# Kernel optimization log

Hardware: AMD Instinct MI355X
Metric: run time of the kernel (lower is better)

## Reference

```python
import jax, jax.numpy as jnp
import numpy as np

INIT_IN = 32      # init_input_dim (raw feature dim of x)
D = 128           # output_dim == init_output_dim
IN_DIM = 2 * D + INIT_IN  # input_dim = 288
NUM_LAYERS = 4    # loop runs num_layers-1 = 3 rounds
NV = 50000        # num variables
NC = 50000        # num constraints
DEG = 16          # padded neighbor list length


def _linear_params(key, out_dim, in_dim):
    k1, k2 = jax.random.split(key)
    bound = 1.0 / np.sqrt(in_dim)
    W = jax.random.uniform(k1, (out_dim, in_dim), minval=-bound, maxval=bound, dtype=jnp.float32)
    b = jax.random.uniform(k2, (out_dim,), minval=-bound, maxval=bound, dtype=jnp.float32)
    return W, b


def setup_inputs() -> dict:
    key = jax.random.key(0)
    ks = jax.random.split(key, 8)
    x = jax.random.normal(ks[0], (NV + NC, INIT_IN), dtype=jnp.float32)
    var_constr_index = jax.random.randint(ks[1], (NV, DEG), 0, NC).astype(jnp.int64)
    constr_var_index = jax.random.randint(ks[2], (NC, DEG), 0, NV).astype(jnp.int64)
    W_iv, b_iv = _linear_params(ks[3], D, INIT_IN)
    W_ic, b_ic = _linear_params(ks[4], D, INIT_IN)
    W_v, b_v = _linear_params(ks[5], D, IN_DIM)
    W_c, b_c = _linear_params(ks[6], D, IN_DIM)
    W_q, b_q = _linear_params(ks[7], 1, 2 * D)
    return dict(x=x, var_constr_index=var_constr_index, constr_var_index=constr_var_index,
                W_iv=W_iv, b_iv=b_iv, W_ic=W_ic, b_ic=b_ic,
                W_v=W_v, b_v=b_v, W_c=W_c, b_c=b_c, W_q=W_q, b_q=b_q)


def reference(x, var_constr_index, constr_var_index,
              W_iv, b_iv, W_ic, b_ic, W_v, b_v, W_c, b_c, W_q, b_q):
    nv = var_constr_index.shape[0]
    var_feat = x[:nv]          # [NV, INIT_IN]
    con_feat = x[nv:]          # [NC, INIT_IN]
    # layer zero init
    lv = var_feat @ W_iv.T + b_iv   # [NV, D]
    lc = con_feat @ W_ic.T + b_ic   # [NC, D]
    zeros = jnp.zeros((1, D), dtype=lv.dtype)
    for _ in range(1, NUM_LAYERS):
        lv_pad = jnp.concatenate([lv, zeros], axis=0)  # -1 pad idx -> zeros row
        lc_pad = jnp.concatenate([lc, zeros], axis=0)
        # constraint update: gather variable neighbors, sum, fuse with linear
        c_agg = lv_pad[constr_var_index].sum(axis=1)   # [NC, D]
        lc_new = jnp.concatenate([c_agg, lc, con_feat], axis=1) @ W_c.T + b_c
        # variable update uses OLD (pre-update) constraint features (lc_pad)
        v_agg = lc_pad[var_constr_index].sum(axis=1)   # [NV, D]
        lv = jnp.concatenate([v_agg, lv, var_feat], axis=1) @ W_v.T + b_v
        lc = lc_new
    # embedding_Q: global sum of variable features broadcast to each variable
    g = lv.sum(axis=0, keepdims=True)                  # [1, D]
    g = jnp.broadcast_to(g, lv.shape)                  # [NV, D]
    Q = jnp.concatenate([g, lv], axis=1) @ W_q.T + b_q # [NV, 1]
    return Q
```

## Files before the change

kernel.cpp:

```cpp
#include <hip/hip_runtime.h>

#define NVV 50000
#define NCC 50000
#define DD 128
#define FIN 32
#define INDIM 288
#define DEG 16

typedef unsigned short u16;
typedef unsigned char u8;
typedef unsigned int u32;
typedef __attribute__((ext_vector_type(8))) short short8;
typedef __attribute__((ext_vector_type(4))) float f32x4;
typedef __attribute__((ext_vector_type(2))) float f32x2;

constexpr int NT = 256;
constexpr int GRID_HALF = 782;

__device__ __forceinline__ float b2f(u16 b) {
  union { u32 u; float f; } v; v.u = ((u32)b) << 16; return v.f;
}
__device__ __forceinline__ u16 f2b(float f) {
  union { float f; u32 u; } v; v.f = f;
  u32 u = v.u + 0x7FFFu + ((v.u >> 16) & 1u);
  return (u16)(u >> 16);
}
__device__ __forceinline__ float bits2f(u32 u) {
  union { u32 u; float f; } v; v.u = u; return v.f;
}
__device__ __forceinline__ u32 pack2(float a, float b) {
  return (u32)f2b(a) | ((u32)f2b(b) << 16);
}
__device__ __forceinline__ u8 f2fp8(float f) {
  return (u8)(__builtin_amdgcn_cvt_pk_fp8_f32(f, f, 0, false) & 0xFF);
}

__device__ __forceinline__ void dma16(const void* g, void* l) {
  __builtin_amdgcn_global_load_lds(
      (__attribute__((address_space(1))) void*)g,
      (__attribute__((address_space(3))) void*)l, 16, 0, 0);
}

__global__ __launch_bounds__(NT) void swizzle_all(
    const float* __restrict__ Wv, const float* __restrict__ Wc,
    const float* __restrict__ Wiv, const float* __restrict__ Wic,
    u16* __restrict__ Wvsw, u16* __restrict__ Wcsw,
    u16* __restrict__ Wivsw, u16* __restrict__ Wicsw)
{
  int t = blockIdx.x * NT + threadIdx.x;
  if (t >= 10240) return;
  const float* W; u16* out; int f; int indim;
  if (t < 4608)       { W = Wv;  out = Wvsw;  f = t;        indim = INDIM; }
  else if (t < 9216)  { W = Wc;  out = Wcsw;  f = t - 4608; indim = INDIM; }
  else if (t < 9728)  { W = Wiv; out = Wivsw; f = t - 9216; indim = FIN; }
  else                { W = Wic; out = Wicsw; f = t - 9728; indim = FIN; }
  int lane = f & 63, nt = (f >> 6) & 7, kt = f >> 9;
  int li = lane & 15, quad = lane >> 4;
  const float* src = W + (size_t)(nt * 16 + li) * indim + kt * 32 + quad * 8;
  float4 a = *(const float4*)src, b = *(const float4*)(src + 4);
  u32 o[4] = { pack2(a.x, a.y), pack2(a.z, a.w), pack2(b.x, b.y), pack2(b.z, b.w) };
  *(int4*)(out + (size_t)f * 8) = *(int4*)o;
}

__global__ __launch_bounds__(NT) void init_fused(
    const float* __restrict__ x,
    const u16* __restrict__ Wivsw, const u16* __restrict__ Wicsw,
    const float* __restrict__ b_iv, const float* __restrict__ b_ic,
    u16* __restrict__ lv0, u16* __restrict__ lc0,
    u8* __restrict__ lv08, u8* __restrict__ lc08,
    u16* __restrict__ xvb, u16* __restrict__ xcb)
{
  __shared__ char smem8[4 * 2048];
  const int bid = blockIdx.x;
  const bool isC = bid >= GRID_HALF;
  const int lb = isC ? bid - GRID_HALF : bid;
  const float* xs = x + (isC ? (size_t)NVV * FIN : 0);
  const u16* Wsw = isC ? Wicsw : Wivsw;
  const float* bias = isC ? b_ic : b_iv;
  u16* out  = isC ? lc0 : lv0;
  u8*  out8 = isC ? lc08 : lv08;
  u16* feat = isC ? xcb : xvb;
  const int nrows = isC ? NCC : NVV;

  const int t = threadIdx.x;
  const int r0 = lb * 64;

  {
    const int row = r0 + (t >> 2);
    if (row < nrows) {
      const float* src = xs + (size_t)row * FIN + (t & 3) * 8;
      float4 a = *(const float4*)src, b = *(const float4*)(src + 4);
      u32 o[4] = { pack2(a.x, a.y), pack2(a.z, a.w), pack2(b.x, b.y), pack2(b.z, b.w) };
      *(int4*)(feat + (size_t)row * FIN + (t & 3) * 8) = *(int4*)o;
    }
  }

  const int wave = t >> 6, l = t & 63;
  const int quad = l >> 4, li = l & 15;
  const int r0w = r0 + wave * 16;
  int rowm = r0w + li;
  if (rowm >= nrows) rowm = nrows - 1;

  short8 afrag;
  {
    const float* src = xs + (size_t)rowm * FIN + quad * 8;
    float4 a = *(const float4*)src, b = *(const float4*)(src + 4);
    u32 o[4] = { pack2(a.x, a.y), pack2(a.z, a.w), pack2(b.x, b.y), pack2(b.z, b.w) };
    afrag = *(short8*)o;
  }

  f32x4 acc[8];
#pragma unroll
  for (int nt = 0; nt < 8; ++nt) acc[nt] = (f32x4){0.f, 0.f, 0.f, 0.f};
#pragma unroll
  for (int nt = 0; nt < 8; ++nt) {
    short8 b = *(const short8*)(Wsw + (size_t)(nt * 64 + l) * 8);
    acc[nt] = __builtin_amdgcn_mfma_f32_16x16x32_bf16(afrag, b, acc[nt], 0, 0, 0);
  }

  u8* s8 = (u8*)(smem8 + wave * 2048);
  const int rbase = r0w + quad * 4;
#pragma unroll
  for (int nt = 0; nt < 8; ++nt) {
    const int col = nt * 16 + li;
    const float bv = bias[col];
#pragma unroll
    for (int i = 0; i < 4; ++i) {
      const int row = rbase + i;
      float v = acc[nt][i] + bv;
      if (row < nrows) out[(size_t)row * DD + col] = f2b(v);
      s8[(quad * 4 + i) * 128 + col] = f2fp8(v);
    }
  }
  asm volatile("s_waitcnt lgkmcnt(0)" ::: "memory");
  if (r0w < nrows) {
    const char* s8c = (const char*)s8 + l * 32;
    char* g8 = (char*)out8 + (size_t)r0w * 128 + l * 32;
#pragma unroll
    for (int c = 0; c < 2; ++c) *(int4*)(g8 + c * 16) = *(const int4*)(s8c + c * 16);
  }
}

__device__ __forceinline__ void issue_group16(const char* gp, int offj, char* slotbase) {
  const char* rp = gp + (size_t)(u32)offj;
#pragma unroll
  for (int k2 = 0; k2 < 4; ++k2)
    dma16(rp + k2 * 64, slotbase + k2 * 1024);
}
__device__ __forceinline__ void consume_slot16(const char* sb, float (&sagg)[4][8]) {
#pragma unroll
  for (int k2 = 0; k2 < 4; ++k2) {
    int4 v = *(const int4*)(sb + k2 * 1024);
    const u32* w = (const u32*)&v;
#pragma unroll
    for (int p = 0; p < 4; ++p) {
      sagg[k2][2 * p]     += bits2f(w[p] << 16);
      sagg[k2][2 * p + 1] += bits2f(w[p] & 0xFFFF0000u);
    }
  }
}
__device__ __forceinline__ void issue_group8(const char* gp, int offj, char* slotbase) {
  const char* rp = gp + (size_t)(u32)offj;
  dma16(rp, slotbase);
  dma16(rp + 64, slotbase + 1024);
}
__device__ __forceinline__ void consume_slot8(const char* slot, int li, int quad,
                                              float (&sagg)[4][8]) {
  const int c2 = quad >> 1, half = quad & 1;
#pragma unroll
  for (int kt = 0; kt < 4; ++kt) {
    int4 v = *(const int4*)(slot + (2 * kt + c2) * 256 + li * 16);
    u32 w0 = half ? (u32)v.z : (u32)v.x;
    u32 w1 = half ? (u32)v.w : (u32)v.y;
    f32x2 a0 = __builtin_amdgcn_cvt_pk_f32_fp8(w0, false);
    f32x2 a1 = __builtin_amdgcn_cvt_pk_f32_fp8(w0, true);
    f32x2 a2 = __builtin_amdgcn_cvt_pk_f32_fp8(w1, false);
    f32x2 a3 = __builtin_amdgcn_cvt_pk_f32_fp8(w1, true);
    sagg[kt][0] += a0.x; sagg[kt][1] += a0.y;
    sagg[kt][2] += a1.x; sagg[kt][3] += a1.y;
    sagg[kt][4] += a2.x; sagg[kt][5] += a2.y;
    sagg[kt][6] += a3.x; sagg[kt][7] += a3.y;
  }
}

template <bool F8, bool W8, bool GACC>
__device__ __forceinline__ void layer_body(
    const void* __restrict__ gsrc, const u16* __restrict__ self,
    const u16* __restrict__ feat, const int* __restrict__ idx,
    const u16* __restrict__ Wsw, const float* __restrict__ bias,
    u16* __restrict__ out, u8* __restrict__ out8, float* __restrict__ g,
    int nrows, int bid, int t, char* smem)
{
  const int wave = t >> 6, l = t & 63;
  const int quad = l >> 4, li = l & 15;
  const int r0w = bid * 64 + wave * 16;

  int4 iv;
  {
    int rload = r0w + (l >> 2);
    if (rload >= nrows) rload = nrows - 1;
    iv = *(const int4*)(idx + (size_t)rload * DEG + (l & 3) * 4);
  }
  int off[DEG];
#pragma unroll
  for (int j = 0; j < DEG; ++j) {
    int comp = ((j & 3) == 0) ? iv.x : ((j & 3) == 1) ? iv.y : ((j & 3) == 2) ? iv.z : iv.w;
    off[j] = __shfl(comp, (li << 2) + (j >> 2)) << (F8 ? 7 : 8);
  }

  int rowm = r0w + li;
  if (rowm >= nrows) rowm = nrows - 1;

  f32x4 acc[8];
#pragma unroll
  for (int nt = 0; nt < 8; ++nt) acc[nt] = (f32x4){0.f, 0.f, 0.f, 0.f};

  {
    short8 a = *(const short8*)(feat + (size_t)rowm * FIN + quad * 8);
#pragma unroll
    for (int nt = 0; nt < 8; ++nt) {
      short8 b = *(const short8*)(Wsw + (size_t)((8 * 8 + nt) * 64 + l) * 8);
      acc[nt] = __builtin_amdgcn_mfma_f32_16x16x32_bf16(a, b, acc[nt], 0, 0, 0);
    }
  }
#pragma unroll
  for (int k2 = 0; k2 < 4; ++k2) {
    short8 a = *(const short8*)(self + (size_t)rowm * DD + k2 * 32 + quad * 8);
#pragma unroll
    for (int nt = 0; nt < 8; ++nt) {
      short8 b = *(const short8*)(Wsw + (size_t)(((4 + k2) * 8 + nt) * 64 + l) * 8);
      acc[nt] = __builtin_amdgcn_mfma_f32_16x16x32_bf16(a, b, acc[nt], 0, 0, 0);
    }
  }

  float sagg[4][8];
#pragma unroll
  for (int k2 = 0; k2 < 4; ++k2)
#pragma unroll
    for (int p = 0; p < 8; ++p) sagg[k2][p] = 0.f;

  asm volatile("s_waitcnt vmcnt(0)" ::: "memory");

  char* wb;
  if constexpr (F8) {
    wb = smem + wave * 8192;
    const char* gp = (const char*)gsrc + quad * 16;
    issue_group8(gp, off[0], wb);
    issue_group8(gp, off[1], wb + 2048);
    issue_group8(gp, off[2], wb + 4096);
    issue_group8(gp, off[3], wb + 6144);
#define R8_STEP(J, IJ)                                               \
    asm volatile("s_waitcnt vmcnt(6)" ::: "memory");                 \
    consume_slot8(wb + ((J) & 3) * 2048, li, quad, sagg);            \
    asm volatile("s_waitcnt lgkmcnt(0)" ::: "memory");               \
    issue_group8(gp, off[IJ], wb + ((J) & 3) * 2048);
#define R8_TAIL(J, VN)                                               \
    asm volatile("s_waitcnt vmcnt(" #VN ")" ::: "memory");           \
    consume_slot8(wb + ((J) & 3) * 2048, li, quad, sagg);
    R8_STEP(0, 4)  R8_STEP(1, 5)  R8_STEP(2, 6)  R8_STEP(3, 7)
    R8_STEP(4, 8)  R8_STEP(5, 9)  R8_STEP(6, 10) R8_STEP(7, 11)
    R8_STEP(8, 12) R8_STEP(9, 13) R8_STEP(10, 14) R8_STEP(11, 15)
    R8_TAIL(12, 6) R8_TAIL(13, 4) R8_TAIL(14, 2)  R8_TAIL(15, 0)
#undef R8_STEP
#undef R8_TAIL
  } else {
    wb = smem + wave * 16384;
    const char* gp = (const char*)gsrc + quad * 16;
    issue_group16(gp, off[0], wb);
    issue_group16(gp, off[1], wb + 4096);
    issue_group16(gp, off[2], wb + 8192);
    issue_group16(gp, off[3], wb + 12288);
#define R16_STEP(J, IJ)                                              \
    asm volatile("s_waitcnt vmcnt(12)" ::: "memory");                \
    consume_slot16(wb + ((J) & 3) * 4096 + l * 16, sagg);            \
    asm volatile("s_waitcnt lgkmcnt(0)" ::: "memory");               \
    issue_group16(gp, off[IJ], wb + ((J) & 3) * 4096);
#define R16_TAIL(J, VN)                                              \
    asm volatile("s_waitcnt vmcnt(" #VN ")" ::: "memory");           \
    consume_slot16(wb + ((J) & 3) * 4096 + l * 16, sagg);
    R16_STEP(0, 4)  R16_STEP(1, 5)  R16_STEP(2, 6)  R16_STEP(3, 7)
    R16_STEP(4, 8)  R16_STEP(5, 9)  R16_STEP(6, 10) R16_STEP(7, 11)
    R16_STEP(8, 12) R16_STEP(9, 13) R16_STEP(10, 14) R16_STEP(11, 15)
    R16_TAIL(12, 12) R16_TAIL(13, 8) R16_TAIL(14, 4) R16_TAIL(15, 0)
#undef R16_STEP
#undef R16_TAIL
  }

#pragma unroll
  for (int k2 = 0; k2 < 4; ++k2) {
    u32 a_bits[4];
#pragma unroll
    for (int p = 0; p < 4; ++p) a_bits[p] = pack2(sagg[k2][2 * p], sagg[k2][2 * p + 1]);
    short8 a = *(short8*)a_bits;
#pragma unroll
    for (int nt = 0; nt < 8; ++nt) {
      short8 b = *(const short8*)(Wsw + (size_t)((k2 * 8 + nt) * 64 + l) * 8);
      acc[nt] = __builtin_amdgcn_mfma_f32_16x16x32_bf16(a, b, acc[nt], 0, 0, 0);
    }
  }

  asm volatile("s_waitcnt lgkmcnt(0)" ::: "memory");
  u8* s8 = (u8*)wb;
  const int rbase = r0w + quad * 4;
  float colsum[8];
#pragma unroll
  for (int nt = 0; nt < 8; ++nt) {
    const int col = nt * 16 + li;
    const float bv = bias[col];
    colsum[nt] = 0.f;
#pragma unroll
    for (int i = 0; i < 4; ++i) {
      const int row = rbase + i;
      float v = acc[nt][i] + bv;
      if (row < nrows) {
        out[(size_t)row * DD + col] = f2b(v);
        if constexpr (GACC) colsum[nt] += v;
      }
      if constexpr (W8) s8[(quad * 4 + i) * 128 + col] = f2fp8(v);
    }
  }
  if constexpr (W8) {
    asm volatile("s_waitcnt lgkmcnt(0)" ::: "memory");
    if (r0w < nrows) {
      const char* s8c = (const char*)s8 + l * 32;
      char* g8 = (char*)out8 + (size_t)r0w * 128 + l * 32;
#pragma unroll
      for (int c = 0; c < 2; ++c) *(int4*)(g8 + c * 16) = *(const int4*)(s8c + c * 16);
    }
  }

  if constexpr (GACC) {
#pragma unroll
    for (int nt = 0; nt < 8; ++nt) {
      colsum[nt] += __shfl_xor(colsum[nt], 16);
      colsum[nt] += __shfl_xor(colsum[nt], 32);
    }
    __syncthreads();
    float* gsum = (float*)smem;
    if (quad == 0) {
#pragma unroll
      for (int nt = 0; nt < 8; ++nt) gsum[wave * 128 + nt * 16 + li] = colsum[nt];
    }
    __syncthreads();
    if (t < 128) {
      float tot = gsum[t] + gsum[128 + t] + gsum[256 + t] + gsum[384 + t];
      atomicAdd(&g[t], tot);
    }
  }
}

template <bool F8, bool W8, bool GACC>
__global__ __launch_bounds__(NT, 2) void layer_merged(
    const void* gsrcC, const u16* selfC, const u16* featC, const int* idxC,
    const u16* WswC, const float* biasC, u16* outC, u8* out8C, int nrowsC,
    const void* gsrcV, const u16* selfV, const u16* featV, const int* idxV,
    const u16* WswV, const float* biasV, u16* outV, u8* out8V, int nrowsV,
    float* g, int c_blocks)
{
  __shared__ char smem[F8 ? 32768 : 65536];
  const int bid = blockIdx.x;
  const int t = threadIdx.x;
  if (bid < c_blocks)
    layer_body<F8, W8, GACC>(gsrcC, selfC, featC, idxC, WswC, biasC, outC, out8C,
                             g, nrowsC, bid, t, smem);
  else
    layer_body<F8, W8, GACC>(gsrcV, selfV, featV, idxV, WswV, biasV, outV, out8V,
                             g, nrowsV, bid - c_blocks, t, smem);
}

__global__ void zero_g(float* g) { g[threadIdx.x] = 0.f; }

__global__ __launch_bounds__(NT) void final_kernel(
    const u16* __restrict__ lv, const float* __restrict__ g,
    const float* __restrict__ Wq, const float* __restrict__ bq,
    float* __restrict__ out)
{
  const int t = threadIdx.x, wave = t >> 6, l = t & 63;
  const float2 wg = *(const float2*)(Wq + 2 * l);
  const float2 wl = *(const float2*)(Wq + DD + 2 * l);
  const float2 gv = *(const float2*)(g + 2 * l);
  float q = wg.x * gv.x + wg.y * gv.y;
#pragma unroll
  for (int off = 32; off; off >>= 1) q += __shfl_down(q, off);
  const float qg = __shfl(q, 0) + bq[0];

  const int r0w = blockIdx.x * 64 + wave * 16;
#pragma unroll
  for (int i = 0; i < 16; ++i) {
    const int r = r0w + i;
    if (r >= NVV) break;
    u32 v = *(const u32*)(lv + (size_t)r * DD + 2 * l);
    float p = wl.x * b2f((u16)(v & 0xFFFF)) + wl.y * b2f((u16)(v >> 16));
#pragma unroll
    for (int off = 32; off; off >>= 1) p += __shfl_down(p, off);
    if (l == 0) out[r] = qg + p;
  }
}

extern "C" void kernel_launch(void* const* d_in, const int* in_sizes, int n_in,
                              void* d_out, int out_size, void* d_ws, size_t ws_size,
                              hipStream_t stream) {
  const float* x    = (const float*)d_in[0];
  const int*   vci  = (const int*)d_in[1];
  const int*   cvi  = (const int*)d_in[2];
  const float* W_iv = (const float*)d_in[3];
  const float* b_iv = (const float*)d_in[4];
  const float* W_ic = (const float*)d_in[5];
  const float* b_ic = (const float*)d_in[6];
  const float* W_v  = (const float*)d_in[7];
  const float* b_v  = (const float*)d_in[8];
  const float* W_c  = (const float*)d_in[9];
  const float* b_c  = (const float*)d_in[10];
  const float* W_q  = (const float*)d_in[11];
  const float* b_q  = (const float*)d_in[12];
  float* out = (float*)d_out;

  float* g = (float*)d_ws;
  u16* base = (u16*)((char*)d_ws + 512);
  const size_t nodef = (size_t)NVV * DD;
  u16* xb    = base;
  u16* Wvsw  = xb + (size_t)(NVV + NCC) * FIN;
  u16* Wcsw  = Wvsw + (size_t)DD * INDIM;
  u16* Wivsw = Wcsw + (size_t)DD * INDIM;
  u16* Wicsw = Wivsw + (size_t)DD * FIN;
  u16* lv0   = Wicsw + (size_t)DD * FIN;
  u16* lc0   = lv0 + nodef;
  u16* lv1   = lc0 + nodef;
  u16* lc1   = lv1 + nodef;
  u8*  lv08  = (u8*)(lc1 + nodef);
  u8*  lc08  = lv08 + nodef;
  u8*  lv18  = lc08 + nodef;
  u8*  lc18  = lv18 + nodef;
  u16* xvb   = xb;
  u16* xcb   = xb + (size_t)NVV * FIN;

  dim3 blk(NT);

  swizzle_all<<<40, blk, 0, stream>>>(W_v, W_c, W_iv, W_ic, Wvsw, Wcsw, Wivsw, Wicsw);
  init_fused<<<2 * GRID_HALF, blk, 0, stream>>>(x, Wivsw, Wicsw, b_iv, b_ic,
                                                lv0, lc0, lv08, lc08, xvb, xcb);
  zero_g<<<1, 128, 0, stream>>>(g);

  layer_merged<true, true, false><<<2 * GRID_HALF, blk, 0, stream>>>(
      lv08, lc0, xcb, cvi, Wcsw, b_c, lc1, lc18, NCC,
      lc08, lv0, xvb, vci, Wvsw, b_v, lv1, lv18, NVV, g, GRID_HALF);
  layer_merged<true, false, false><<<2 * GRID_HALF, blk, 0, stream>>>(
      lv18, lc1, xcb, cvi, Wcsw, b_c, lc0, nullptr, NCC,
      lc18, lv1, xvb, vci, Wvsw, b_v, lv0, nullptr, NVV, g, GRID_HALF);
  layer_merged<false, false, true><<<GRID_HALF, blk, 0, stream>>>(
      lv0, lc0, xcb, cvi, Wcsw, b_c, lc1, nullptr, NCC,
      lc0, lv0, xvb, vci, Wvsw, b_v, lv1, nullptr, NVV, g, 0);

  final_kernel<<<GRID_HALF, blk, 0, stream>>>(lv1, g, W_q, b_q, out);
}
```

Before: 325.7 us.

## Use fp8 gathers in last layer, stage stores via LDS with nontemporal writes

```diff
diff --git a/kernel.cpp b/kernel.cpp
--- a/kernel.cpp
+++ b/kernel.cpp
@@ -13,6 +13,7 @@
 typedef __attribute__((ext_vector_type(8))) short short8;
 typedef __attribute__((ext_vector_type(4))) float f32x4;
 typedef __attribute__((ext_vector_type(2))) float f32x2;
+typedef __attribute__((ext_vector_type(4))) unsigned int u32x4;
 
 constexpr int NT = 256;
 constexpr int GRID_HALF = 782;
@@ -40,15 +41,25 @@
       (__attribute__((address_space(1))) void*)g,
       (__attribute__((address_space(3))) void*)l, 16, 0, 0);
 }
+__device__ __forceinline__ short8 ntload8(const u16* p) {
+  return __builtin_nontemporal_load((const short8*)p);
+}
+__device__ __forceinline__ void ntstore16(void* p, u32x4 v) {
+  __builtin_nontemporal_store(v, (u32x4*)p);
+}
 
 __global__ __launch_bounds__(NT) void swizzle_all(
     const float* __restrict__ Wv, const float* __restrict__ Wc,
     const float* __restrict__ Wiv, const float* __restrict__ Wic,
     u16* __restrict__ Wvsw, u16* __restrict__ Wcsw,
-    u16* __restrict__ Wivsw, u16* __restrict__ Wicsw)
+    u16* __restrict__ Wivsw, u16* __restrict__ Wicsw, float* __restrict__ g)
 {
   int t = blockIdx.x * NT + threadIdx.x;
-  if (t >= 10240) return;
+  if (t >= 10240) {
+    int gi = t - 10240;
+    if (gi < 128) g[gi] = 0.f;
+    return;
+  }
   const float* W; u16* out; int f; int indim;
   if (t < 4608)       { W = Wv;  out = Wvsw;  f = t;        indim = INDIM; }
   else if (t < 9216)  { W = Wc;  out = Wcsw;  f = t - 4608; indim = INDIM; }
@@ -58,8 +69,8 @@
   int li = lane & 15, quad = lane >> 4;
   const float* src = W + (size_t)(nt * 16 + li) * indim + kt * 32 + quad * 8;
   float4 a = *(const float4*)src, b = *(const float4*)(src + 4);
-  u32 o[4] = { pack2(a.x, a.y), pack2(a.z, a.w), pack2(b.x, b.y), pack2(b.z, b.w) };
-  *(int4*)(out + (size_t)f * 8) = *(int4*)o;
+  u32x4 o = { pack2(a.x, a.y), pack2(a.z, a.w), pack2(b.x, b.y), pack2(b.z, b.w) };
+  *(u32x4*)(out + (size_t)f * 8) = o;
 }
 
 __global__ __launch_bounds__(NT) void init_fused(
@@ -70,7 +81,7 @@
     u8* __restrict__ lv08, u8* __restrict__ lc08,
     u16* __restrict__ xvb, u16* __restrict__ xcb)
 {
-  __shared__ char smem8[4 * 2048];
+  __shared__ char smem[4 * 8192];
   const int bid = blockIdx.x;
   const bool isC = bid >= GRID_HALF;
   const int lb = isC ? bid - GRID_HALF : bid;
@@ -90,8 +101,8 @@
     if (row < nrows) {
       const float* src = xs + (size_t)row * FIN + (t & 3) * 8;
       float4 a = *(const float4*)src, b = *(const float4*)(src + 4);
-      u32 o[4] = { pack2(a.x, a.y), pack2(a.z, a.w), pack2(b.x, b.y), pack2(b.z, b.w) };
-      *(int4*)(feat + (size_t)row * FIN + (t & 3) * 8) = *(int4*)o;
+      u32x4 o = { pack2(a.x, a.y), pack2(a.z, a.w), pack2(b.x, b.y), pack2(b.z, b.w) };
+      ntstore16(feat + (size_t)row * FIN + (t & 3) * 8, o);
     }
   }
 
@@ -105,8 +116,8 @@
   {
     const float* src = xs + (size_t)rowm * FIN + quad * 8;
     float4 a = *(const float4*)src, b = *(const float4*)(src + 4);
-    u32 o[4] = { pack2(a.x, a.y), pack2(a.z, a.w), pack2(b.x, b.y), pack2(b.z, b.w) };
-    afrag = *(short8*)o;
+    u32x4 o = { pack2(a.x, a.y), pack2(a.z, a.w), pack2(b.x, b.y), pack2(b.z, b.w) };
+    afrag = *(short8*)&o;
   }
 
   f32x4 acc[8];
@@ -118,47 +129,33 @@
     acc[nt] = __builtin_amdgcn_mfma_f32_16x16x32_bf16(afrag, b, acc[nt], 0, 0, 0);
   }
 
-  u8* s8 = (u8*)(smem8 + wave * 2048);
-  const int rbase = r0w + quad * 4;
+  char* wb = smem + wave * 8192;
+  u16* swt = (u16*)wb;
+  u8*  s8  = (u8*)(wb + 4096);
 #pragma unroll
   for (int nt = 0; nt < 8; ++nt) {
     const int col = nt * 16 + li;
     const float bv = bias[col];
 #pragma unroll
     for (int i = 0; i < 4; ++i) {
-      const int row = rbase + i;
       float v = acc[nt][i] + bv;
-      if (row < nrows) out[(size_t)row * DD + col] = f2b(v);
+      swt[(quad * 4 + i) * 128 + col] = f2b(v);
       s8[(quad * 4 + i) * 128 + col] = f2fp8(v);
     }
   }
   asm volatile("s_waitcnt lgkmcnt(0)" ::: "memory");
   if (r0w < nrows) {
+    const char* sc = (const char*)swt + l * 64;
+    char* g16 = (char*)out + (size_t)r0w * 256 + l * 64;
+#pragma unroll
+    for (int c = 0; c < 4; ++c) ntstore16(g16 + c * 16, *(const u32x4*)(sc + c * 16));
     const char* s8c = (const char*)s8 + l * 32;
     char* g8 = (char*)out8 + (size_t)r0w * 128 + l * 32;
 #pragma unroll
-    for (int c = 0; c < 2; ++c) *(int4*)(g8 + c * 16) = *(const int4*)(s8c + c * 16);
-  }
-}
-
-__device__ __forceinline__ void issue_group16(const char* gp, int offj, char* slotbase) {
-  const char* rp = gp + (size_t)(u32)offj;
-#pragma unroll
-  for (int k2 = 0; k2 < 4; ++k2)
-    dma16(rp + k2 * 64, slotbase + k2 * 1024);
-}
-__device__ __forceinline__ void consume_slot16(const char* sb, float (&sagg)[4][8]) {
-#pragma unroll
-  for (int k2 = 0; k2 < 4; ++k2) {
-    int4 v = *(const int4*)(sb + k2 * 1024);
-    const u32* w = (const u32*)&v;
-#pragma unroll
-    for (int p = 0; p < 4; ++p) {
-      sagg[k2][2 * p]     += bits2f(w[p] << 16);
-      sagg[k2][2 * p + 1] += bits2f(w[p] & 0xFFFF0000u);
-    }
-  }
-}
+    for (int c = 0; c < 2; ++c) ntstore16(g8 + c * 16, *(const u32x4*)(s8c + c * 16));
+  }
+}
+
 __device__ __forceinline__ void issue_group8(const char* gp, int offj, char* slotbase) {
   const char* rp = gp + (size_t)(u32)offj;
   dma16(rp, slotbase);
@@ -183,9 +180,9 @@
   }
 }
 
-template <bool F8, bool W8, bool GACC>
+template <bool GACC>
 __device__ __forceinline__ void layer_body(
-    const void* __restrict__ gsrc, const u16* __restrict__ self,
+    const u8* __restrict__ gsrc, const u16* __restrict__ self,
     const u16* __restrict__ feat, const int* __restrict__ idx,
     const u16* __restrict__ Wsw, const float* __restrict__ bias,
     u16* __restrict__ out, u8* __restrict__ out8, float* __restrict__ g,
@@ -205,7 +202,7 @@
 #pragma unroll
   for (int j = 0; j < DEG; ++j) {
     int comp = ((j & 3) == 0) ? iv.x : ((j & 3) == 1) ? iv.y : ((j & 3) == 2) ? iv.z : iv.w;
-    off[j] = __shfl(comp, (li << 2) + (j >> 2)) << (F8 ? 7 : 8);
+    off[j] = __shfl(comp, (li << 2) + (j >> 2)) << 7;
   }
 
   int rowm = r0w + li;
@@ -216,7 +213,7 @@
   for (int nt = 0; nt < 8; ++nt) acc[nt] = (f32x4){0.f, 0.f, 0.f, 0.f};
 
   {
-    short8 a = *(const short8*)(feat + (size_t)rowm * FIN + quad * 8);
+    short8 a = ntload8(feat + (size_t)rowm * FIN + quad * 8);
 #pragma unroll
     for (int nt = 0; nt < 8; ++nt) {
       short8 b = *(const short8*)(Wsw + (size_t)((8 * 8 + nt) * 64 + l) * 8);
@@ -225,7 +222,7 @@
   }
 #pragma unroll
   for (int k2 = 0; k2 < 4; ++k2) {
-    short8 a = *(const short8*)(self + (size_t)rowm * DD + k2 * 32 + quad * 8);
+    short8 a = ntload8(self + (size_t)rowm * DD + k2 * 32 + quad * 8);
 #pragma unroll
     for (int nt = 0; nt < 8; ++nt) {
       short8 b = *(const short8*)(Wsw + (size_t)(((4 + k2) * 8 + nt) * 64 + l) * 8);
@@ -241,50 +238,26 @@
 
   asm volatile("s_waitcnt vmcnt(0)" ::: "memory");
 
-  char* wb;
-  if constexpr (F8) {
-    wb = smem + wave * 8192;
-    const char* gp = (const char*)gsrc + quad * 16;
-    issue_group8(gp, off[0], wb);
-    issue_group8(gp, off[1], wb + 2048);
-    issue_group8(gp, off[2], wb + 4096);
-    issue_group8(gp, off[3], wb + 6144);
+  char* wb = smem + wave * 8192;
+  const char* gp = (const char*)gsrc + quad * 16;
+  issue_group8(gp, off[0], wb);
+  issue_group8(gp, off[1], wb + 2048);
+  issue_group8(gp, off[2], wb + 4096);
+  issue_group8(gp, off[3], wb + 6144);
 #define R8_STEP(J, IJ)                                               \
-    asm volatile("s_waitcnt vmcnt(6)" ::: "memory");                 \
-    consume_slot8(wb + ((J) & 3) * 2048, li, quad, sagg);            \
-    asm volatile("s_waitcnt lgkmcnt(0)" ::: "memory");               \
-    issue_group8(gp, off[IJ], wb + ((J) & 3) * 2048);
+  asm volatile("s_waitcnt vmcnt(6)" ::: "memory");                   \
+  consume_slot8(wb + ((J) & 3) * 2048, li, quad, sagg);              \
+  asm volatile("s_waitcnt lgkmcnt(0)" ::: "memory");                 \
+  issue_group8(gp, off[IJ], wb + ((J) & 3) * 2048);
 #define R8_TAIL(J, VN)                                               \
-    asm volatile("s_waitcnt vmcnt(" #VN ")" ::: "memory");           \
-    consume_slot8(wb + ((J) & 3) * 2048, li, quad, sagg);
-    R8_STEP(0, 4)  R8_STEP(1, 5)  R8_STEP(2, 6)  R8_STEP(3, 7)
-    R8_STEP(4, 8)  R8_STEP(5, 9)  R8_STEP(6, 10) R8_STEP(7, 11)
-    R8_STEP(8, 12) R8_STEP(9, 13) R8_STEP(10, 14) R8_STEP(11, 15)
-    R8_TAIL(12, 6) R8_TAIL(13, 4) R8_TAIL(14, 2)  R8_TAIL(15, 0)
+  asm volatile("s_waitcnt vmcnt(" #VN ")" ::: "memory");             \
+  consume_slot8(wb + ((J) & 3) * 2048, li, quad, sagg);
+  R8_STEP(0, 4)  R8_STEP(1, 5)  R8_STEP(2, 6)  R8_STEP(3, 7)
+  R8_STEP(4, 8)  R8_STEP(5, 9)  R8_STEP(6, 10) R8_STEP(7, 11)
+  R8_STEP(8, 12) R8_STEP(9, 13) R8_STEP(10, 14) R8_STEP(11, 15)
+  R8_TAIL(12, 6) R8_TAIL(13, 4) R8_TAIL(14, 2)  R8_TAIL(15, 0)
 #undef R8_STEP
 #undef R8_TAIL
-  } else {
-    wb = smem + wave * 16384;
-    const char* gp = (const char*)gsrc + quad * 16;
-    issue_group16(gp, off[0], wb);
-    issue_group16(gp, off[1], wb + 4096);
-    issue_group16(gp, off[2], wb + 8192);
-    issue_group16(gp, off[3], wb + 12288);
-#define R16_STEP(J, IJ)                                              \
-    asm volatile("s_waitcnt vmcnt(12)" ::: "memory");                \
-    consume_slot16(wb + ((J) & 3) * 4096 + l * 16, sagg);            \
-    asm volatile("s_waitcnt lgkmcnt(0)" ::: "memory");               \
-    issue_group16(gp, off[IJ], wb + ((J) & 3) * 4096);
-#define R16_TAIL(J, VN)                                              \
-    asm volatile("s_waitcnt vmcnt(" #VN ")" ::: "memory");           \
-    consume_slot16(wb + ((J) & 3) * 4096 + l * 16, sagg);
-    R16_STEP(0, 4)  R16_STEP(1, 5)  R16_STEP(2, 6)  R16_STEP(3, 7)
-    R16_STEP(4, 8)  R16_STEP(5, 9)  R16_STEP(6, 10) R16_STEP(7, 11)
-    R16_STEP(8, 12) R16_STEP(9, 13) R16_STEP(10, 14) R16_STEP(11, 15)
-    R16_TAIL(12, 12) R16_TAIL(13, 8) R16_TAIL(14, 4) R16_TAIL(15, 0)
-#undef R16_STEP
-#undef R16_TAIL
-  }
 
 #pragma unroll
   for (int k2 = 0; k2 < 4; ++k2) {
@@ -300,8 +273,9 @@
   }
 
   asm volatile("s_waitcnt lgkmcnt(0)" ::: "memory");
-  u8* s8 = (u8*)wb;
-  const int rbase = r0w + quad * 4;
+  u16* swt = (u16*)wb;
+  u8*  s8  = (u8*)(wb + 4096);
+  const bool wvalid = (r0w < nrows);
   float colsum[8];
 #pragma unroll
   for (int nt = 0; nt < 8; ++nt) {
@@ -310,26 +284,31 @@
     colsum[nt] = 0.f;
 #pragma unroll
     for (int i = 0; i < 4; ++i) {
-      const int row = rbase + i;
       float v = acc[nt][i] + bv;
-      if (row < nrows) {
-        out[(size_t)row * DD + col] = f2b(v);
-        if constexpr (GACC) colsum[nt] += v;
-      }
-      if constexpr (W8) s8[(quad * 4 + i) * 128 + col] = f2fp8(v);
-    }
-  }
-  if constexpr (W8) {
-    asm volatile("s_waitcnt lgkmcnt(0)" ::: "memory");
-    if (r0w < nrows) {
+      swt[(quad * 4 + i) * 128 + col] = f2b(v);
+      if (out8) s8[(quad * 4 + i) * 128 + col] = f2fp8(v);
+      if constexpr (GACC) colsum[nt] += v;
+    }
+  }
+  asm volatile("s_waitcnt lgkmcnt(0)" ::: "memory");
+  if (wvalid) {
+    const char* sc = (const char*)swt + l * 64;
+    char* g16 = (char*)out + (size_t)r0w * 256 + l * 64;
+#pragma unroll
+    for (int c = 0; c < 4; ++c) ntstore16(g16 + c * 16, *(const u32x4*)(sc + c * 16));
+    if (out8) {
       const char* s8c = (const char*)s8 + l * 32;
       char* g8 = (char*)out8 + (size_t)r0w * 128 + l * 32;
 #pragma unroll
-      for (int c = 0; c < 2; ++c) *(int4*)(g8 + c * 16) = *(const int4*)(s8c + c * 16);
+      for (int c = 0; c < 2; ++c) ntstore16(g8 + c * 16, *(const u32x4*)(s8c + c * 16));
     }
   }
 
   if constexpr (GACC) {
+    if (!wvalid) {
+#pragma unroll
+      for (int nt = 0; nt < 8; ++nt) colsum[nt] = 0.f;
+    }
 #pragma unroll
     for (int nt = 0; nt < 8; ++nt) {
       colsum[nt] += __shfl_xor(colsum[nt], 16);
@@ -349,26 +328,24 @@
   }
 }
 
-template <bool F8, bool W8, bool GACC>
+template <bool GACC>
 __global__ __launch_bounds__(NT, 2) void layer_merged(
-    const void* gsrcC, const u16* selfC, const u16* featC, const int* idxC,
+    const u8* gsrcC, const u16* selfC, const u16* featC, const int* idxC,
     const u16* WswC, const float* biasC, u16* outC, u8* out8C, int nrowsC,
-    const void* gsrcV, const u16* selfV, const u16* featV, const int* idxV,
+    const u8* gsrcV, const u16* selfV, const u16* featV, const int* idxV,
     const u16* WswV, const float* biasV, u16* outV, u8* out8V, int nrowsV,
     float* g, int c_blocks)
 {
-  __shared__ char smem[F8 ? 32768 : 65536];
+  __shared__ char smem[32768];
   const int bid = blockIdx.x;
   const int t = threadIdx.x;
   if (bid < c_blocks)
-    layer_body<F8, W8, GACC>(gsrcC, selfC, featC, idxC, WswC, biasC, outC, out8C,
-                             g, nrowsC, bid, t, smem);
+    layer_body<GACC>(gsrcC, selfC, featC, idxC, WswC, biasC, outC, out8C,
+                     g, nrowsC, bid, t, smem);
   else
-    layer_body<F8, W8, GACC>(gsrcV, selfV, featV, idxV, WswV, biasV, outV, out8V,
-                             g, nrowsV, bid - c_blocks, t, smem);
-}
-
-__global__ void zero_g(float* g) { g[threadIdx.x] = 0.f; }
+    layer_body<GACC>(gsrcV, selfV, featV, idxV, WswV, biasV, outV, out8V,
+                     g, nrowsV, bid - c_blocks, t, smem);
+}
 
 __global__ __launch_bounds__(NT) void final_kernel(
     const u16* __restrict__ lv, const float* __restrict__ g,
@@ -431,25 +408,25 @@
   u8*  lc08  = lv08 + nodef;
   u8*  lv18  = lc08 + nodef;
   u8*  lc18  = lv18 + nodef;
+  u8*  lc28  = lv08;
   u16* xvb   = xb;
   u16* xcb   = xb + (size_t)NVV * FIN;
 
   dim3 blk(NT);
 
-  swizzle_all<<<40, blk, 0, stream>>>(W_v, W_c, W_iv, W_ic, Wvsw, Wcsw, Wivsw, Wicsw);
+  swizzle_all<<<41, blk, 0, stream>>>(W_v, W_c, W_iv, W_ic, Wvsw, Wcsw, Wivsw, Wicsw, g);
   init_fused<<<2 * GRID_HALF, blk, 0, stream>>>(x, Wivsw, Wicsw, b_iv, b_ic,
                                                 lv0, lc0, lv08, lc08, xvb, xcb);
-  zero_g<<<1, 128, 0, stream>>>(g);
-
-  layer_merged<true, true, false><<<2 * GRID_HALF, blk, 0, stream>>>(
+
+  layer_merged<false><<<2 * GRID_HALF, blk, 0, stream>>>(
       lv08, lc0, xcb, cvi, Wcsw, b_c, lc1, lc18, NCC,
       lc08, lv0, xvb, vci, Wvsw, b_v, lv1, lv18, NVV, g, GRID_HALF);
-  layer_merged<true, false, false><<<2 * GRID_HALF, blk, 0, stream>>>(
-      lv18, lc1, xcb, cvi, Wcsw, b_c, lc0, nullptr, NCC,
+  layer_merged<false><<<2 * GRID_HALF, blk, 0, stream>>>(
+      lv18, lc1, xcb, cvi, Wcsw, b_c, lc0, lc28, NCC,
       lc18, lv1, xvb, vci, Wvsw, b_v, lv0, nullptr, NVV, g, GRID_HALF);
-  layer_merged<false, false, true><<<GRID_HALF, blk, 0, stream>>>(
-      lv0, lc0, xcb, cvi, Wcsw, b_c, lc1, nullptr, NCC,
-      lc0, lv0, xvb, vci, Wvsw, b_v, lv1, nullptr, NVV, g, 0);
+  layer_merged<true><<<GRID_HALF, blk, 0, stream>>>(
+      lc28, lv0, xvb, vci, Wvsw, b_v, lv1, nullptr, NVV,
+      lc28, lv0, xvb, vci, Wvsw, b_v, lv1, nullptr, NVV, g, 0);
 
   final_kernel<<<GRID_HALF, blk, 0, stream>>>(lv1, g, W_q, b_q, out);
 }
```

New measurement: 340.9 us. 1.05x slower.
